# Kernel tuning notes

Hardware: AMD Instinct MI355X
Metric: run time of the kernel (lower is better)

Reference implementation:

```python
import jax, jax.numpy as jnp
import numpy as np

N_NODES = 100000
N_EDGES = 3200000
K = 10
ALPHA = 0.1


def setup_inputs() -> dict:
    key = jax.random.key(0)
    k1, k2, k3, k4 = jax.random.split(key, 4)
    x = jax.random.normal(k1, (N_NODES, 512), dtype=jnp.float32)
    edge_index = jax.random.randint(k2, (2, N_EDGES), 0, N_NODES, dtype=jnp.int64)
    W1 = jax.random.normal(k3, (512, 16), dtype=jnp.float32) * 0.05
    b1 = jnp.zeros((16,), dtype=jnp.float32)
    W2 = jax.random.normal(k4, (16, 64), dtype=jnp.float32) * 0.05
    b2 = jnp.zeros((64,), dtype=jnp.float32)
    return {"x": x, "W1": W1, "b1": b1, "W2": W2, "b2": b2,
            "edge_index": edge_index}


def reference(x, W1, b1, W2, b2, edge_index):
    n = x.shape[0]
    # MLP encoder
    h = jax.nn.relu(x @ W1 + b1)          # [N, 16]
    h = h @ W2 + b2                       # [N, C]
    # gcn_norm with self-loops (PyG default for APPNP)
    self_idx = jnp.arange(n, dtype=edge_index.dtype)
    row = jnp.concatenate([edge_index[0], self_idx])   # source nodes
    col = jnp.concatenate([edge_index[1], self_idx])   # target nodes
    deg = jax.ops.segment_sum(jnp.ones_like(col, dtype=h.dtype), col, num_segments=n)
    dinv = jnp.where(deg > 0, jax.lax.rsqrt(deg), 0.0)
    norm = dinv[row] * dinv[col]          # [E+N]
    # APPNP: K steps of x <- (1-a) * A_hat x + a * x0
    h0 = h
    def step(h, _):
        agg = jax.ops.segment_sum(norm[:, None] * h[row], col, num_segments=n)
        return (1.0 - ALPHA) * agg + ALPHA * h0, None
    h, _ = jax.lax.scan(step, h, None, length=K)
    return jax.nn.log_softmax(h, axis=1)
```

## Files before the change

### kernel.cpp

```cpp
#include <hip/hip_runtime.h>
#include <hip/hip_bf16.h>


typedef unsigned short u16;
typedef __attribute__((ext_vector_type(8))) short short8;
typedef __attribute__((ext_vector_type(4))) float f32x4;

#define WPB 4
#define BSH2 9
#define BN2 512
#define NBMAX 200
#define CAP 20480
#define SCWG 392

__device__ __forceinline__ float loadF(const void* p, size_t i, int bf) {
  if (bf) return __bfloat162float(((const __hip_bfloat16*)p)[i]);
  return ((const float*)p)[i];
}
__device__ __forceinline__ float blo(unsigned u) {
  return __uint_as_float(u << 16);
}
__device__ __forceinline__ float bhi(unsigned u) {
  return __uint_as_float(u & 0xffff0000u);
}
__device__ __forceinline__ u16 f2b(float v) {
  __hip_bfloat16 b = __float2bfloat16(v);
  return *reinterpret_cast<u16*>(&b);
}
__device__ __forceinline__ unsigned pk2(float lo, float hi) {
  return (unsigned)f2b(lo) | ((unsigned)f2b(hi) << 16);
}
__device__ __forceinline__ int clampN(int v, int N) {
  v = v < 0 ? 0 : v;
  return v >= N ? N - 1 : v;
}

__global__ void detect_k(const void* x, const int* ei, int* flags) {
  __shared__ int red[2];
  const int tid = threadIdx.x;
  if (tid < 2) red[tid] = 0;
  __syncthreads();
  const __hip_bfloat16* xb = (const __hip_bfloat16*)x;
  float v = __bfloat162float(xb[tid]);
  int sane = (v == v && fabsf(v) < 64.f) ? 1 : 0;
  int zer = (ei[2 * tid + 1] == 0) ? 1 : 0;
  atomicAdd(&red[0], sane);
  atomicAdd(&red[1], zer);
  __syncthreads();
  if (tid == 0) {
    flags[0] = (red[0] >= 1024 - 32) ? 1 : 0;
    flags[1] = (red[1] >= 1024 - 128) ? 1 : 0;
  }
}

__global__ __launch_bounds__(256) void scat_k(
    const int* __restrict__ ei, int E, int N, int NB,
    int* __restrict__ gcur, uint2* __restrict__ bpair,
    const int* __restrict__ flags) {
  __shared__ int hist[NBMAX];
  __shared__ int resv[NBMAX];
  const int tid = threadIdx.x;
  const int chunk = (E + SCWG - 1) / SCWG;
  const int e0 = blockIdx.x * chunk;
  const int e1 = min(e0 + chunk, E);
  if (e0 >= E) return;
  const int wide = flags[1];
  for (int i = tid; i < NB; i += 256) hist[i] = 0;
  __syncthreads();
  for (int e = e0 + tid; e < e1; e += 256) {
    int c = wide ? ei[2 * ((long)E + e)] : ei[(long)E + e];
    atomicAdd(&hist[clampN(c, N) >> BSH2], 1);
  }
  __syncthreads();
  for (int b = tid; b < NB; b += 256) {
    int cnt = hist[b];
    resv[b] = cnt ? atomicAdd(&gcur[b], cnt) : 0;
  }
  __syncthreads();
  for (int i = tid; i < NB; i += 256) hist[i] = 0;
  __syncthreads();
  for (int e = e0 + tid; e < e1; e += 256) {
    int r = wide ? ei[2 * (long)e] : ei[e];
    int c = wide ? ei[2 * ((long)E + e)] : ei[(long)E + e];
    r = clampN(r, N); c = clampN(c, N);
    const int b = c >> BSH2;
    const int pos = resv[b] + atomicAdd(&hist[b], 1);
    if (pos < CAP)
      bpair[(size_t)b * CAP + pos] = make_uint2((unsigned)r, (unsigned)c);
  }
}

__global__ void bscan_k(const int* __restrict__ gcur, int NB,
                        int* __restrict__ cbase) {
  if (threadIdx.x == 0) {
    int s = 0;
    for (int b = 0; b < NB; b++) {
      cbase[b] = s;
      s += min(gcur[b], CAP);
    }
    cbase[NB] = s;
  }
}

__global__ __launch_bounds__(1024) void fill2a_k(
    const uint2* __restrict__ bpair, const int* __restrict__ gcur,
    const int* __restrict__ cbase, int* __restrict__ colptr,
    float* __restrict__ dinv, int N, int NB) {
  __shared__ int lhist[BN2];
  __shared__ int pref[BN2];
  const int b = blockIdx.x;
  const int tid = threadIdx.x;
  const int nb0 = b << BSH2;
  const int nn = min(BN2, N - nb0);
  if (tid < BN2) lhist[tid] = 0;
  __syncthreads();
  const size_t wbeg = (size_t)b * CAP;
  const int cnt = min(gcur[b], CAP);
  for (int i = tid; i < cnt; i += 1024) {
    int dl = (int)bpair[wbeg + i].y - nb0;
    atomicAdd(&lhist[dl], 1);
  }
  __syncthreads();
  if (tid < BN2) pref[tid] = lhist[tid];
  __syncthreads();
  for (int off = 1; off < BN2; off <<= 1) {
    int v = 0;
    if (tid < BN2 && tid >= off) v = pref[tid - off];
    __syncthreads();
    if (tid < BN2) pref[tid] += v;
    __syncthreads();
  }
  if (tid < nn) {
    const int excl = pref[tid] - lhist[tid];
    colptr[nb0 + tid] = cbase[b] + excl;
    dinv[nb0 + tid] = rsqrtf(1.0f + (float)lhist[tid]);
  }
  if (b == NB - 1 && tid == 0) colptr[N] = cbase[NB];
}

__global__ __launch_bounds__(1024) void fill2b_k(
    const uint2* __restrict__ bpair, const int* __restrict__ gcur,
    const int* __restrict__ colptr, const float* __restrict__ dinv,
    uint2* __restrict__ srow2, int N, int NB) {
  __shared__ int lcur[BN2];
  __shared__ float ldv[BN2];
  const int b = blockIdx.x;
  const int tid = threadIdx.x;
  const int nb0 = b << BSH2;
  const int nn = min(BN2, N - nb0);
  if (tid < nn) {
    lcur[tid] = colptr[nb0 + tid];
    ldv[tid] = dinv[nb0 + tid];
  }
  __syncthreads();
  const size_t wbeg = (size_t)b * CAP;
  const int cnt = min(gcur[b], CAP);
  for (int i = tid; i < cnt; i += 1024) {
    const uint2 p = bpair[wbeg + i];
    const int dl = (int)p.y - nb0;
    const int slot = atomicAdd(&lcur[dl], 1);
    const float nrm = dinv[p.x] * ldv[dl];
    srow2[slot] = make_uint2(p.x, __float_as_uint(nrm));
  }
}

__global__ __launch_bounds__(256) void mlp_k(
    const void* __restrict__ x, const void* __restrict__ W1,
    const void* __restrict__ b1, const void* __restrict__ W2,
    const void* __restrict__ b2, const int* __restrict__ flags,
    u16* __restrict__ h0, u16* __restrict__ ping, int N) {
  __shared__ __align__(16) short Blds[8192];
  __shared__ float W2s[16 * 64];
  __shared__ float b1s[16];
  __shared__ float b2s[64];
  __shared__ float h1s[WPB][16][17];

  const int tid = threadIdx.x;
  const int f0 = flags[0];

  for (int idx = tid; idx < 8192; idx += 256) {
    int ks = idx >> 9, ln = (idx >> 3) & 63, j = idx & 7;
    int k = ks * 32 + ((ln >> 4) << 3) + j;
    int n = ln & 15;
    float w = loadF(W1, (size_t)k * 16 + n, f0);
    Blds[idx] = (short)f2b(w);
  }
  for (int idx = tid; idx < 1024; idx += 256) W2s[idx] = loadF(W2, idx, f0);
  if (tid < 16) b1s[tid] = loadF(b1, tid, f0);
  else if (tid >= 64 && tid < 128) b2s[tid - 64] = loadF(b2, tid - 64, f0);
  __syncthreads();

  const int lane = tid & 63;
  const int wv = tid >> 6;
  const int tile = (blockIdx.x * WPB + wv) * 16;
  if (tile >= N) return;

  const int m = lane & 15;
  const int quad = lane >> 4;
  const int row = min(tile + m, N - 1);
  const size_t rowbase = (size_t)row * 512 + (quad << 3);

  f32x4 acc = {0.f, 0.f, 0.f, 0.f};
#pragma unroll
  for (int ks = 0; ks < 16; ks++) {
    short8 a;
    if (f0) {
      a = *reinterpret_cast<const short8*>((const u16*)x + rowbase + ks * 32);
    } else {
      const float* xf = (const float*)x + rowbase + ks * 32;
      const float4 lo = *reinterpret_cast<const float4*>(xf);
      const float4 hi = *reinterpret_cast<const float4*>(xf + 4);
      a[0] = (short)f2b(lo.x); a[1] = (short)f2b(lo.y);
      a[2] = (short)f2b(lo.z); a[3] = (short)f2b(lo.w);
      a[4] = (short)f2b(hi.x); a[5] = (short)f2b(hi.y);
      a[6] = (short)f2b(hi.z); a[7] = (short)f2b(hi.w);
    }
    const short8 bf = *reinterpret_cast<const short8*>(&Blds[(ks * 64 + lane) * 8]);
    acc = __builtin_amdgcn_mfma_f32_16x16x32_bf16(a, bf, acc, 0, 0, 0);
  }

#pragma unroll
  for (int r = 0; r < 4; r++)
    h1s[wv][quad * 4 + r][m] = fmaxf(acc[r] + b1s[m], 0.f);

  for (int mm = 0; mm < 16; mm++) {
    const int node = tile + mm;
    if (node >= N) break;
    float hh = b2s[lane];
#pragma unroll
    for (int j = 0; j < 16; j++) hh += h1s[wv][mm][j] * W2s[(j << 6) + lane];
    const u16 u = f2b(hh);
    const size_t o = (size_t)node * 64 + lane;
    h0[o] = u;
    ping[o] = u;
  }
}

#define EDGE_FMA(acc0, acc1, acc2, acc3, acc4, acc5, acc6, acc7, ee, uu)      \
  {                                                                           \
    const float nn_ = __uint_as_float((ee).y);                                \
    acc0 = fmaf(nn_, blo((uu).x), acc0); acc1 = fmaf(nn_, bhi((uu).x), acc1); \
    acc2 = fmaf(nn_, blo((uu).y), acc2); acc3 = fmaf(nn_, bhi((uu).y), acc3); \
    acc4 = fmaf(nn_, blo((uu).z), acc4); acc5 = fmaf(nn_, bhi((uu).z), acc5); \
    acc6 = fmaf(nn_, blo((uu).w), acc6); acc7 = fmaf(nn_, bhi((uu).w), acc7); \
  }

__global__ __launch_bounds__(256) void gather_k(
    const u16* __restrict__ hcur, const u16* __restrict__ h0,
    const int* __restrict__ colptr, const uint2* __restrict__ srow2,
    const float* __restrict__ dinv, u16* __restrict__ hnext, int N) {
  const int gw = (int)((blockIdx.x * 256u + threadIdx.x) >> 6);
  if (gw >= N) return;
  const int lane = threadIdx.x & 63;
  const int o = lane >> 3, s = lane & 7;
  const int soff = s << 3;
  const int beg = __builtin_amdgcn_readfirstlane(colptr[gw]);
  const int end = __builtin_amdgcn_readfirstlane(colptr[gw + 1]);
  const float di = dinv[gw];

  float a0 = 0.f, a1 = 0.f, a2 = 0.f, a3 = 0.f;
  float a4 = 0.f, a5 = 0.f, a6 = 0.f, a7 = 0.f;
  float c0 = 0.f, c1 = 0.f, c2 = 0.f, c3 = 0.f;
  float c4 = 0.f, c5 = 0.f, c6 = 0.f, c7 = 0.f;
  int t = beg + o;
  for (; t + 24 < end; t += 32) {
    const uint2 e0 = srow2[t];
    const uint2 e1 = srow2[t + 8];
    const uint2 e2 = srow2[t + 16];
    const uint2 e3 = srow2[t + 24];
    const uint4 u0 = *reinterpret_cast<const uint4*>(hcur + (((size_t)e0.x) << 6) + soff);
    const uint4 u1 = *reinterpret_cast<const uint4*>(hcur + (((size_t)e1.x) << 6) + soff);
    const uint4 u2 = *reinterpret_cast<const uint4*>(hcur + (((size_t)e2.x) << 6) + soff);
    const uint4 u3 = *reinterpret_cast<const uint4*>(hcur + (((size_t)e3.x) << 6) + soff);
    EDGE_FMA(a0, a1, a2, a3, a4, a5, a6, a7, e0, u0);
    EDGE_FMA(c0, c1, c2, c3, c4, c5, c6, c7, e1, u1);
    EDGE_FMA(a0, a1, a2, a3, a4, a5, a6, a7, e2, u2);
    EDGE_FMA(c0, c1, c2, c3, c4, c5, c6, c7, e3, u3);
  }
  for (; t + 8 < end; t += 16) {
    const uint2 e0 = srow2[t];
    const uint2 e1 = srow2[t + 8];
    const uint4 u0 = *reinterpret_cast<const uint4*>(hcur + (((size_t)e0.x) << 6) + soff);
    const uint4 u1 = *reinterpret_cast<const uint4*>(hcur + (((size_t)e1.x) << 6) + soff);
    EDGE_FMA(a0, a1, a2, a3, a4, a5, a6, a7, e0, u0);
    EDGE_FMA(c0, c1, c2, c3, c4, c5, c6, c7, e1, u1);
  }
  if (t < end) {
    const uint2 e0 = srow2[t];
    const uint4 u0 = *reinterpret_cast<const uint4*>(hcur + (((size_t)e0.x) << 6) + soff);
    EDGE_FMA(a0, a1, a2, a3, a4, a5, a6, a7, e0, u0);
  }
  a0 += c0; a1 += c1; a2 += c2; a3 += c3;
  a4 += c4; a5 += c5; a6 += c6; a7 += c7;
#pragma unroll
  for (int d = 8; d < 64; d <<= 1) {
    a0 += __shfl_xor(a0, d, 64); a1 += __shfl_xor(a1, d, 64);
    a2 += __shfl_xor(a2, d, 64); a3 += __shfl_xor(a3, d, 64);
    a4 += __shfl_xor(a4, d, 64); a5 += __shfl_xor(a5, d, 64);
    a6 += __shfl_xor(a6, d, 64); a7 += __shfl_xor(a7, d, 64);
  }

  const size_t base = (((size_t)gw) << 6) + soff;
  const uint4 hs = *reinterpret_cast<const uint4*>(hcur + base);
  const uint4 hz = *reinterpret_cast<const uint4*>(h0 + base);
  const float dd = di * di;
  const float r0 = 0.9f * (a0 + dd * blo(hs.x)) + 0.1f * blo(hz.x);
  const float r1 = 0.9f * (a1 + dd * bhi(hs.x)) + 0.1f * bhi(hz.x);
  const float r2 = 0.9f * (a2 + dd * blo(hs.y)) + 0.1f * blo(hz.y);
  const float r3 = 0.9f * (a3 + dd * bhi(hs.y)) + 0.1f * bhi(hz.y);
  const float r4 = 0.9f * (a4 + dd * blo(hs.z)) + 0.1f * blo(hz.z);
  const float r5 = 0.9f * (a5 + dd * bhi(hs.z)) + 0.1f * bhi(hz.z);
  const float r6 = 0.9f * (a6 + dd * blo(hs.w)) + 0.1f * blo(hz.w);
  const float r7 = 0.9f * (a7 + dd * bhi(hs.w)) + 0.1f * bhi(hz.w);
  if (o == 0) {
    uint4 pv;
    pv.x = pk2(r0, r1); pv.y = pk2(r2, r3);
    pv.z = pk2(r4, r5); pv.w = pk2(r6, r7);
    *reinterpret_cast<uint4*>(hnext + base) = pv;
  }
}

__global__ __launch_bounds__(256) void lsm_k(const u16* __restrict__ hin,
                                             void* __restrict__ out,
                                             const int* __restrict__ flags, int N) {
  const int gw = (int)((blockIdx.x * 256u + threadIdx.x) >> 6);
  if (gw >= N) return;
  const int lane = threadIdx.x & 63;
  const size_t o = (((size_t)gw) << 6) + lane;
  const float v = __bfloat162float(*reinterpret_cast<const __hip_bfloat16*>(&hin[o]));
  float m = v;
#pragma unroll
  for (int off = 32; off; off >>= 1) m = fmaxf(m, __shfl_xor(m, off, 64));
  float e = __expf(v - m);
  float ssum = e;
#pragma unroll
  for (int off = 32; off; off >>= 1) ssum += __shfl_xor(ssum, off, 64);
  const float r = v - m - __logf(ssum);
  if (flags[0]) ((__hip_bfloat16*)out)[o] = __float2bfloat16(r);
  else ((float*)out)[o] = r;
}

extern "C" void kernel_launch(void* const* d_in, const int* in_sizes, int n_in,
                              void* d_out, int out_size, void* d_ws, size_t ws_size,
                              hipStream_t stream) {
  (void)n_in; (void)out_size; (void)ws_size;
  const void* x  = d_in[0];
  const void* W1 = d_in[1];
  const void* b1 = d_in[2];
  const void* W2 = d_in[3];
  const void* b2 = d_in[4];
  const int* ei  = (const int*)d_in[5];

  const int N = in_sizes[0] / 512;
  const int E = in_sizes[5] / 2;
  const int NB = (N + BN2 - 1) >> BSH2;

  char* w = (char*)d_ws;
  size_t off = 0;
  auto alloc = [&](size_t bytes) -> void* {
    void* p = w + off;
    off += (bytes + 255) & ~(size_t)255;
    return p;
  };
  const size_t hb = (size_t)N * 64 * 2;
  const size_t bpb = (size_t)NB * CAP * 8;
  char*  regionA = (char*)alloc(2 * hb > bpb ? 2 * hb : bpb);
  u16*   h0     = (u16*)regionA;
  u16*   ping   = (u16*)(regionA + hb);
  uint2* bpair  = (uint2*)regionA;
  uint2* srow2  = (uint2*)alloc((size_t)E * 8);
  int*   colptr = (int*)alloc(((size_t)N + 1) * 4);
  float* dinv   = (float*)alloc((size_t)N * 4);
  int*   gcur   = (int*)alloc((size_t)NB * 4);
  int*   cbase  = (int*)alloc(((size_t)NB + 1) * 4);
  int*   flags  = (int*)alloc(256);
  u16*   pong   = (u16*)d_out;

  hipMemsetAsync(gcur, 0, (size_t)NB * 4, stream);
  detect_k<<<1, 1024, 0, stream>>>(x, ei, flags);
  scat_k<<<SCWG, 256, 0, stream>>>(ei, E, N, NB, gcur, bpair, flags);
  bscan_k<<<1, 64, 0, stream>>>(gcur, NB, cbase);
  fill2a_k<<<NB, 1024, 0, stream>>>(bpair, gcur, cbase, colptr, dinv, N, NB);
  fill2b_k<<<NB, 1024, 0, stream>>>(bpair, gcur, colptr, dinv, srow2, N, NB);
  mlp_k<<<(N + 63) / 64, 256, 0, stream>>>(x, W1, b1, W2, b2, flags, h0, ping, N);

  const int gblocks = (N + WPB - 1) / WPB;
  for (int it = 0; it < 10; ++it) {
    if ((it & 1) == 0)
      gather_k<<<gblocks, 256, 0, stream>>>(ping, h0, colptr, srow2, dinv, pong, N);
    else
      gather_k<<<gblocks, 256, 0, stream>>>(pong, h0, colptr, srow2, dinv, ping, N);
  }
  lsm_k<<<gblocks, 256, 0, stream>>>(ping, d_out, flags, N);
}
```

Before: 1.080 ms.

## Split features into 16-wide planes and pack edges into 32-bit words

The hidden state is stored as four planes of 16 channels each. The gather kernel gets a second grid dimension over planes, so each 16-lane group handles one node's 16-channel slice, with 8 edge slots and two halves per lane. Each edge record shrinks from 8 bytes to 4: a 17-bit source index plus a 15-bit fp16 norm, which drops the sign bit. The aim is to shrink the edge stream and to keep each gathered plane small enough to cache well. In exchange, every edge is read four times (once per plane), the norm loses precision, and the packing assumes node ids below 2^17.

```diff
diff --git a/kernel.cpp b/kernel.cpp
--- a/kernel.cpp
+++ b/kernel.cpp
@@ -1,10 +1,12 @@
 #include <hip/hip_runtime.h>
 #include <hip/hip_bf16.h>
+#include <hip/hip_fp16.h>
 
 
 typedef unsigned short u16;
 typedef __attribute__((ext_vector_type(8))) short short8;
 typedef __attribute__((ext_vector_type(4))) float f32x4;
+typedef __attribute__((ext_vector_type(4))) unsigned u32x4;
 
 #define WPB 4
 #define BSH2 9
@@ -141,7 +143,7 @@
 __global__ __launch_bounds__(1024) void fill2b_k(
     const uint2* __restrict__ bpair, const int* __restrict__ gcur,
     const int* __restrict__ colptr, const float* __restrict__ dinv,
-    uint2* __restrict__ srow2, int N, int NB) {
+    unsigned* __restrict__ epk, int N, int NB) {
   __shared__ int lcur[BN2];
   __shared__ float ldv[BN2];
   const int b = blockIdx.x;
@@ -160,7 +162,7 @@
     const int dl = (int)p.y - nb0;
     const int slot = atomicAdd(&lcur[dl], 1);
     const float nrm = dinv[p.x] * ldv[dl];
-    srow2[slot] = make_uint2(p.x, __float_as_uint(nrm));
+    epk[slot] = (p.x << 15) | (unsigned)__half_as_ushort(__float2half(nrm));
   }
 }
 
@@ -201,12 +203,20 @@
   const size_t rowbase = (size_t)row * 512 + (quad << 3);
 
   f32x4 acc = {0.f, 0.f, 0.f, 0.f};
-#pragma unroll
-  for (int ks = 0; ks < 16; ks++) {
-    short8 a;
-    if (f0) {
-      a = *reinterpret_cast<const short8*>((const u16*)x + rowbase + ks * 32);
-    } else {
+  if (f0) {
+    short8 af[16];
+#pragma unroll
+    for (int ks = 0; ks < 16; ks++)
+      af[ks] = *reinterpret_cast<const short8*>((const u16*)x + rowbase + ks * 32);
+#pragma unroll
+    for (int ks = 0; ks < 16; ks++) {
+      const short8 bf = *reinterpret_cast<const short8*>(&Blds[(ks * 64 + lane) * 8]);
+      acc = __builtin_amdgcn_mfma_f32_16x16x32_bf16(af[ks], bf, acc, 0, 0, 0);
+    }
+  } else {
+#pragma unroll
+    for (int ks = 0; ks < 16; ks++) {
+      short8 a;
       const float* xf = (const float*)x + rowbase + ks * 32;
       const float4 lo = *reinterpret_cast<const float4*>(xf);
       const float4 hi = *reinterpret_cast<const float4*>(xf + 4);
@@ -214,9 +224,9 @@
       a[2] = (short)f2b(lo.z); a[3] = (short)f2b(lo.w);
       a[4] = (short)f2b(hi.x); a[5] = (short)f2b(hi.y);
       a[6] = (short)f2b(hi.z); a[7] = (short)f2b(hi.w);
+      const short8 bf = *reinterpret_cast<const short8*>(&Blds[(ks * 64 + lane) * 8]);
+      acc = __builtin_amdgcn_mfma_f32_16x16x32_bf16(a, bf, acc, 0, 0, 0);
     }
-    const short8 bf = *reinterpret_cast<const short8*>(&Blds[(ks * 64 + lane) * 8]);
-    acc = __builtin_amdgcn_mfma_f32_16x16x32_bf16(a, bf, acc, 0, 0, 0);
   }
 
 #pragma unroll
@@ -230,93 +240,72 @@
 #pragma unroll
     for (int j = 0; j < 16; j++) hh += h1s[wv][mm][j] * W2s[(j << 6) + lane];
     const u16 u = f2b(hh);
-    const size_t o = (size_t)node * 64 + lane;
+    const size_t o = ((size_t)(lane >> 4) * N + node) * 16 + (lane & 15);
     h0[o] = u;
     ping[o] = u;
   }
 }
 
-#define EDGE_FMA(acc0, acc1, acc2, acc3, acc4, acc5, acc6, acc7, ee, uu)      \
-  {                                                                           \
-    const float nn_ = __uint_as_float((ee).y);                                \
-    acc0 = fmaf(nn_, blo((uu).x), acc0); acc1 = fmaf(nn_, bhi((uu).x), acc1); \
-    acc2 = fmaf(nn_, blo((uu).y), acc2); acc3 = fmaf(nn_, bhi((uu).y), acc3); \
-    acc4 = fmaf(nn_, blo((uu).z), acc4); acc5 = fmaf(nn_, bhi((uu).z), acc5); \
-    acc6 = fmaf(nn_, blo((uu).w), acc6); acc7 = fmaf(nn_, bhi((uu).w), acc7); \
-  }
-
 __global__ __launch_bounds__(256) void gather_k(
     const u16* __restrict__ hcur, const u16* __restrict__ h0,
-    const int* __restrict__ colptr, const uint2* __restrict__ srow2,
+    const int* __restrict__ colptr, const unsigned* __restrict__ epk,
     const float* __restrict__ dinv, u16* __restrict__ hnext, int N) {
-  const int gw = (int)((blockIdx.x * 256u + threadIdx.x) >> 6);
+  const int p = blockIdx.y;
+  const int lane = threadIdx.x & 63;
+  const int wv = threadIdx.x >> 6;
+  const int grp = lane >> 4;
+  const int l16 = lane & 15;
+  const int es = l16 >> 1;
+  const int ho = (l16 & 1) << 3;
+  const int gw = blockIdx.x * 16 + wv * 4 + grp;
   if (gw >= N) return;
-  const int lane = threadIdx.x & 63;
-  const int o = lane >> 3, s = lane & 7;
-  const int soff = s << 3;
-  const int beg = __builtin_amdgcn_readfirstlane(colptr[gw]);
-  const int end = __builtin_amdgcn_readfirstlane(colptr[gw + 1]);
-  const float di = dinv[gw];
+  const u16* __restrict__ hp = hcur + (((size_t)p * N) << 4);
+  const int beg = colptr[gw];
+  const int end = colptr[gw + 1];
 
   float a0 = 0.f, a1 = 0.f, a2 = 0.f, a3 = 0.f;
   float a4 = 0.f, a5 = 0.f, a6 = 0.f, a7 = 0.f;
-  float c0 = 0.f, c1 = 0.f, c2 = 0.f, c3 = 0.f;
-  float c4 = 0.f, c5 = 0.f, c6 = 0.f, c7 = 0.f;
-  int t = beg + o;
-  for (; t + 24 < end; t += 32) {
-    const uint2 e0 = srow2[t];
-    const uint2 e1 = srow2[t + 8];
-    const uint2 e2 = srow2[t + 16];
-    const uint2 e3 = srow2[t + 24];
-    const uint4 u0 = *reinterpret_cast<const uint4*>(hcur + (((size_t)e0.x) << 6) + soff);
-    const uint4 u1 = *reinterpret_cast<const uint4*>(hcur + (((size_t)e1.x) << 6) + soff);
-    const uint4 u2 = *reinterpret_cast<const uint4*>(hcur + (((size_t)e2.x) << 6) + soff);
-    const uint4 u3 = *reinterpret_cast<const uint4*>(hcur + (((size_t)e3.x) << 6) + soff);
-    EDGE_FMA(a0, a1, a2, a3, a4, a5, a6, a7, e0, u0);
-    EDGE_FMA(c0, c1, c2, c3, c4, c5, c6, c7, e1, u1);
-    EDGE_FMA(a0, a1, a2, a3, a4, a5, a6, a7, e2, u2);
-    EDGE_FMA(c0, c1, c2, c3, c4, c5, c6, c7, e3, u3);
-  }
-  for (; t + 8 < end; t += 16) {
-    const uint2 e0 = srow2[t];
-    const uint2 e1 = srow2[t + 8];
-    const uint4 u0 = *reinterpret_cast<const uint4*>(hcur + (((size_t)e0.x) << 6) + soff);
-    const uint4 u1 = *reinterpret_cast<const uint4*>(hcur + (((size_t)e1.x) << 6) + soff);
-    EDGE_FMA(a0, a1, a2, a3, a4, a5, a6, a7, e0, u0);
-    EDGE_FMA(c0, c1, c2, c3, c4, c5, c6, c7, e1, u1);
-  }
-  if (t < end) {
-    const uint2 e0 = srow2[t];
-    const uint4 u0 = *reinterpret_cast<const uint4*>(hcur + (((size_t)e0.x) << 6) + soff);
-    EDGE_FMA(a0, a1, a2, a3, a4, a5, a6, a7, e0, u0);
-  }
-  a0 += c0; a1 += c1; a2 += c2; a3 += c3;
-  a4 += c4; a5 += c5; a6 += c6; a7 += c7;
-#pragma unroll
-  for (int d = 8; d < 64; d <<= 1) {
+  int slot = beg + es;
+  while (__any(slot < end)) {
+    if (slot < end) {
+      const unsigned e = __builtin_nontemporal_load(epk + slot);
+      const float n =
+          __half2float(__ushort_as_half((unsigned short)(e & 0x7fffu)));
+      const u32x4 u = *reinterpret_cast<const u32x4*>(
+          hp + (((size_t)(e >> 15)) << 4) + ho);
+      a0 = fmaf(n, blo(u[0]), a0); a1 = fmaf(n, bhi(u[0]), a1);
+      a2 = fmaf(n, blo(u[1]), a2); a3 = fmaf(n, bhi(u[1]), a3);
+      a4 = fmaf(n, blo(u[2]), a4); a5 = fmaf(n, bhi(u[2]), a5);
+      a6 = fmaf(n, blo(u[3]), a6); a7 = fmaf(n, bhi(u[3]), a7);
+    }
+    slot += 8;
+  }
+#pragma unroll
+  for (int d = 2; d <= 8; d <<= 1) {
     a0 += __shfl_xor(a0, d, 64); a1 += __shfl_xor(a1, d, 64);
     a2 += __shfl_xor(a2, d, 64); a3 += __shfl_xor(a3, d, 64);
     a4 += __shfl_xor(a4, d, 64); a5 += __shfl_xor(a5, d, 64);
     a6 += __shfl_xor(a6, d, 64); a7 += __shfl_xor(a7, d, 64);
   }
-
-  const size_t base = (((size_t)gw) << 6) + soff;
-  const uint4 hs = *reinterpret_cast<const uint4*>(hcur + base);
-  const uint4 hz = *reinterpret_cast<const uint4*>(h0 + base);
-  const float dd = di * di;
-  const float r0 = 0.9f * (a0 + dd * blo(hs.x)) + 0.1f * blo(hz.x);
-  const float r1 = 0.9f * (a1 + dd * bhi(hs.x)) + 0.1f * bhi(hz.x);
-  const float r2 = 0.9f * (a2 + dd * blo(hs.y)) + 0.1f * blo(hz.y);
-  const float r3 = 0.9f * (a3 + dd * bhi(hs.y)) + 0.1f * bhi(hz.y);
-  const float r4 = 0.9f * (a4 + dd * blo(hs.z)) + 0.1f * blo(hz.z);
-  const float r5 = 0.9f * (a5 + dd * bhi(hs.z)) + 0.1f * bhi(hz.z);
-  const float r6 = 0.9f * (a6 + dd * blo(hs.w)) + 0.1f * blo(hz.w);
-  const float r7 = 0.9f * (a7 + dd * bhi(hs.w)) + 0.1f * bhi(hz.w);
-  if (o == 0) {
-    uint4 pv;
-    pv.x = pk2(r0, r1); pv.y = pk2(r2, r3);
-    pv.z = pk2(r4, r5); pv.w = pk2(r6, r7);
-    *reinterpret_cast<uint4*>(hnext + base) = pv;
+  if (es == 0) {
+    const size_t base = (((size_t)p * N + gw) << 4) + ho;
+    const u32x4 hs = *reinterpret_cast<const u32x4*>(hcur + base);
+    const u32x4 hz =
+        __builtin_nontemporal_load(reinterpret_cast<const u32x4*>(h0 + base));
+    const float di = dinv[gw];
+    const float dd = di * di;
+    const float r0 = 0.9f * (a0 + dd * blo(hs[0])) + 0.1f * blo(hz[0]);
+    const float r1 = 0.9f * (a1 + dd * bhi(hs[0])) + 0.1f * bhi(hz[0]);
+    const float r2 = 0.9f * (a2 + dd * blo(hs[1])) + 0.1f * blo(hz[1]);
+    const float r3 = 0.9f * (a3 + dd * bhi(hs[1])) + 0.1f * bhi(hz[1]);
+    const float r4 = 0.9f * (a4 + dd * blo(hs[2])) + 0.1f * blo(hz[2]);
+    const float r5 = 0.9f * (a5 + dd * bhi(hs[2])) + 0.1f * bhi(hz[2]);
+    const float r6 = 0.9f * (a6 + dd * blo(hs[3])) + 0.1f * blo(hz[3]);
+    const float r7 = 0.9f * (a7 + dd * bhi(hs[3])) + 0.1f * bhi(hz[3]);
+    u32x4 pv;
+    pv[0] = pk2(r0, r1); pv[1] = pk2(r2, r3);
+    pv[2] = pk2(r4, r5); pv[3] = pk2(r6, r7);
+    __builtin_nontemporal_store(pv, reinterpret_cast<u32x4*>(hnext + base));
   }
 }
 
@@ -326,8 +315,8 @@
   const int gw = (int)((blockIdx.x * 256u + threadIdx.x) >> 6);
   if (gw >= N) return;
   const int lane = threadIdx.x & 63;
-  const size_t o = (((size_t)gw) << 6) + lane;
-  const float v = __bfloat162float(*reinterpret_cast<const __hip_bfloat16*>(&hin[o]));
+  const size_t oin = ((size_t)(lane >> 4) * N + gw) * 16 + (lane & 15);
+  const float v = __bfloat162float(*reinterpret_cast<const __hip_bfloat16*>(&hin[oin]));
   float m = v;
 #pragma unroll
   for (int off = 32; off; off >>= 1) m = fmaxf(m, __shfl_xor(m, off, 64));
@@ -336,6 +325,7 @@
 #pragma unroll
   for (int off = 32; off; off >>= 1) ssum += __shfl_xor(ssum, off, 64);
   const float r = v - m - __logf(ssum);
+  const size_t o = (((size_t)gw) << 6) + lane;
   if (flags[0]) ((__hip_bfloat16*)out)[o] = __float2bfloat16(r);
   else ((float*)out)[o] = r;
 }
@@ -368,7 +358,7 @@
   u16*   h0     = (u16*)regionA;
   u16*   ping   = (u16*)(regionA + hb);
   uint2* bpair  = (uint2*)regionA;
-  uint2* srow2  = (uint2*)alloc((size_t)E * 8);
+  unsigned* epk = (unsigned*)alloc((size_t)E * 4);
   int*   colptr = (int*)alloc(((size_t)N + 1) * 4);
   float* dinv   = (float*)alloc((size_t)N * 4);
   int*   gcur   = (int*)alloc((size_t)NB * 4);
@@ -381,15 +371,16 @@
   scat_k<<<SCWG, 256, 0, stream>>>(ei, E, N, NB, gcur, bpair, flags);
   bscan_k<<<1, 64, 0, stream>>>(gcur, NB, cbase);
   fill2a_k<<<NB, 1024, 0, stream>>>(bpair, gcur, cbase, colptr, dinv, N, NB);
-  fill2b_k<<<NB, 1024, 0, stream>>>(bpair, gcur, colptr, dinv, srow2, N, NB);
+  fill2b_k<<<NB, 1024, 0, stream>>>(bpair, gcur, colptr, dinv, epk, N, NB);
   mlp_k<<<(N + 63) / 64, 256, 0, stream>>>(x, W1, b1, W2, b2, flags, h0, ping, N);
 
-  const int gblocks = (N + WPB - 1) / WPB;
+  const int gpb = (N + 15) >> 4;
+  dim3 ggrid(gpb, 4);
   for (int it = 0; it < 10; ++it) {
     if ((it & 1) == 0)
-      gather_k<<<gblocks, 256, 0, stream>>>(ping, h0, colptr, srow2, dinv, pong, N);
+      gather_k<<<ggrid, 256, 0, stream>>>(ping, h0, colptr, epk, dinv, pong, N);
     else
-      gather_k<<<gblocks, 256, 0, stream>>>(pong, h0, colptr, srow2, dinv, ping, N);
-  }
-  lsm_k<<<gblocks, 256, 0, stream>>>(ping, d_out, flags, N);
-}
+      gather_k<<<ggrid, 256, 0, stream>>>(pong, h0, colptr, epk, dinv, ping, N);
+  }
+  lsm_k<<<(N + WPB - 1) / WPB, 256, 0, stream>>>(ping, d_out, flags, N);
+}
```

Measured after the change: 1.611 ms. 1.49x slower.
